# Kernel optimization log

Measured on AMD Instinct MI355X. Metric: run time of the kernel, lower is better.

The kernel has to match this reference:

```python
import jax, jax.numpy as jnp
import numpy as np

NUM_HEAD = 16
D_MODEL = 1024
D_HEAD = D_MODEL // NUM_HEAD
BATCH = 4
SEQ = 2048


def setup_inputs() -> dict:
    key = jax.random.key(0)
    kq, kk, kv, kw, kb = jax.random.split(key, 5)
    Q = jax.random.normal(kq, (BATCH, SEQ, D_MODEL), dtype=jnp.float32)
    K = jax.random.normal(kk, (BATCH, SEQ, D_MODEL), dtype=jnp.float32)
    V = jax.random.normal(kv, (BATCH, SEQ, D_MODEL), dtype=jnp.float32)
    # nn.Linear weight [out, in] and bias [out]; scaled like torch default init
    Wq_w = jax.random.normal(kw, (D_MODEL, D_MODEL), dtype=jnp.float32) * (1.0 / np.sqrt(D_MODEL))
    Wq_b = jax.random.normal(kb, (D_MODEL,), dtype=jnp.float32) * 0.01
    return {"Q": Q, "K": K, "V": V, "Wq_w": Wq_w, "Wq_b": Wq_b}


def _split_head(x):
    # [b, s, d_model] -> [b, h, s, d_head]
    b, s, _ = x.shape
    return x.reshape(b, s, NUM_HEAD, D_HEAD).transpose(0, 2, 1, 3)


def reference(Q, K, V, Wq_w, Wq_b):
    # NOTE: original module (faithfully) uses Wq for all three projections.
    q = Q @ Wq_w.T + Wq_b
    k = K @ Wq_w.T + Wq_b
    v = V @ Wq_w.T + Wq_b
    q = _split_head(q)  # [b, h, s, dh]
    k = _split_head(k)
    v = _split_head(v)
    scale = 1.0 / jnp.sqrt(jnp.float32(D_HEAD))
    scores = jnp.einsum("bhqd,bhkd->bhqk", q, k) * scale  # [b, h, s, s]
    att_w = jax.nn.softmax(scores, axis=-1)
    out = jnp.einsum("bhqk,bhkd->bhqd", att_w, v)
    out = out.transpose(0, 2, 1, 3).reshape(Q.shape[0], -1, D_MODEL)
    return out, att_w
```

## Files before the change

kernel.cpp:

```cpp
#include <hip/hip_runtime.h>

typedef _Float16 f16;
typedef _Float16 f16x8 __attribute__((ext_vector_type(8)));
typedef _Float16 f16x4 __attribute__((ext_vector_type(4)));
typedef float    f32x4 __attribute__((ext_vector_type(4)));

static constexpr int NBATCH = 4;
static constexpr int NH     = 16;
static constexpr int SQ     = 2048;
static constexpr int DM     = 1024;
static constexpr int DHEAD  = 64;
static constexpr size_t TEL = (size_t)NBATCH * SQ * DM;
static constexpr size_t WEL = (size_t)DM * DM;

#define MFMA(a, b, c) __builtin_amdgcn_mfma_f32_16x16x32_f16((a), (b), (c), 0, 0, 0)

#define GLOAD_LDS16(g, l)                                        \
    __builtin_amdgcn_global_load_lds(                            \
        (const __attribute__((address_space(1))) void*)(g),      \
        (__attribute__((address_space(3))) void*)(l), 16, 0, 0)

__global__ __launch_bounds__(256) void cvt_kernel(
    const float* __restrict__ X0, const float* __restrict__ X1,
    const float* __restrict__ X2, const float* __restrict__ W,
    f16* __restrict__ y0, f16* __restrict__ y1,
    f16* __restrict__ y2, f16* __restrict__ yw)
{
    constexpr int CX = (int)(TEL / 8);
    constexpr int CW = (int)(WEL / 8);
    const int total = 3 * CX + CW;
    for (int c = blockIdx.x * blockDim.x + threadIdx.x; c < total;
         c += gridDim.x * blockDim.x) {
        const float* src; f16* dst; int off;
        if (c < CX)            { src = X0; dst = y0; off = c; }
        else if (c < 2 * CX)   { src = X1; dst = y1; off = c - CX; }
        else if (c < 3 * CX)   { src = X2; dst = y2; off = c - 2 * CX; }
        else                   { src = W;  dst = yw; off = c - 3 * CX; }
        const float* p = src + (size_t)off * 8;
        float4 lo = *(const float4*)p;
        float4 hi = *(const float4*)(p + 4);
        f16x8 v;
        v[0] = (f16)lo.x; v[1] = (f16)lo.y; v[2] = (f16)lo.z; v[3] = (f16)lo.w;
        v[4] = (f16)hi.x; v[5] = (f16)hi.y; v[6] = (f16)hi.z; v[7] = (f16)hi.w;
        *(f16x8*)(dst + (size_t)off * 8) = v;
    }
}

__global__ __launch_bounds__(256, 2) void proj_kernel(
    const f16* __restrict__ X0, const f16* __restrict__ X1,
    const f16* __restrict__ X2, const f16* __restrict__ W,
    const float* __restrict__ bias,
    f16* __restrict__ wq, f16* __restrict__ wk, f16* __restrict__ wv)
{
    alignas(16) __shared__ f16 la[2][128 * 32];
    alignas(16) __shared__ f16 lb[2][128 * 32];

    const int bid   = blockIdx.x;
    const int which = bid / 512;
    const int t0    = bid % 512;
    const int nb    = t0 >> 6;
    const int mb    = t0 & 63;
    const f16* __restrict__ X  = (which == 0) ? X0 : (which == 1) ? X1 : X2;
    const f16* __restrict__ A0 = X + (size_t)mb * 128 * DM;
    const f16* __restrict__ B0 = W + (size_t)nb * 128 * DM;

    const int tid  = threadIdx.x;
    const int wave = tid >> 6;
    const int lane = tid & 63;
    const int wr   = wave >> 1, wc = wave & 1;
    const int l16  = lane & 15, g = lane >> 4;
    const int m_base = mb * 128 + wr * 64;
    const int n_base = nb * 128 + wc * 64;

    auto stage = [&](int buf, int k0) {
        #pragma unroll
        for (int half = 0; half < 2; ++half) {
            const int idx = half * 256 + wave * 64 + lane;
            const int row = idx >> 2;
            const int sc  = (idx & 3) ^ ((row >> 1) & 3);
            const int db  = (half * 256 + wave * 64) * 8;
            GLOAD_LDS16(A0 + (size_t)row * DM + k0 + sc * 8, &la[buf][db]);
            GLOAD_LDS16(B0 + (size_t)row * DM + k0 + sc * 8, &lb[buf][db]);
        }
    };

    f32x4 acc[4][4];
    #pragma unroll
    for (int i = 0; i < 4; ++i)
        #pragma unroll
        for (int j = 0; j < 4; ++j)
            acc[i][j] = (f32x4){0.f, 0.f, 0.f, 0.f};

    stage(0, 0);
    __syncthreads();
    for (int t = 0; t < 32; ++t) {
        const int buf = t & 1;
        if (t < 31) stage(buf ^ 1, (t + 1) * 32);
        f16x8 af[4], bf[4];
        #pragma unroll
        for (int qs = 0; qs < 4; ++qs) {
            const int row = wr * 64 + qs * 16 + l16;
            af[qs] = *(const f16x8*)&la[buf][row * 32 +
                                             ((g ^ ((row >> 1) & 3)) << 3)];
        }
        #pragma unroll
        for (int ns = 0; ns < 4; ++ns) {
            const int row = wc * 64 + ns * 16 + l16;
            bf[ns] = *(const f16x8*)&lb[buf][row * 32 +
                                             ((g ^ ((row >> 1) & 3)) << 3)];
        }
        #pragma unroll
        for (int qs = 0; qs < 4; ++qs)
            #pragma unroll
            for (int ns = 0; ns < 4; ++ns)
                acc[qs][ns] = MFMA(af[qs], bf[ns], acc[qs][ns]);
        __syncthreads();
    }

    const int    s_base = m_base & (SQ - 1);
    const int    b      = m_base >> 11;
    const int    h      = nb * 2 + wc;
    const size_t bh     = (size_t)b * NH + h;

    float bv[4];
    #pragma unroll
    for (int ns = 0; ns < 4; ++ns) bv[ns] = bias[n_base + ns * 16 + l16];

    if (which == 2) {
        #pragma unroll
        for (int qs = 0; qs < 4; ++qs)
            #pragma unroll
            for (int ns = 0; ns < 4; ++ns) {
                f16x4 pk;
                #pragma unroll
                for (int r = 0; r < 4; ++r) pk[r] = (f16)(acc[qs][ns][r] + bv[ns]);
                const int dh = ns * 16 + l16;
                const int s0 = s_base + qs * 16 + 4 * g;
                *(f16x4*)(wv + (bh * DHEAD + dh) * SQ + s0) = pk;
            }
    } else {
        f16* __restrict__ dst = (which == 0) ? wq : wk;
        const float sc = (which == 0) ? 0.125f : 1.0f;
        #pragma unroll
        for (int qs = 0; qs < 4; ++qs)
            #pragma unroll
            for (int ns = 0; ns < 4; ++ns)
                #pragma unroll
                for (int r = 0; r < 4; ++r) {
                    const int s  = s_base + qs * 16 + 4 * g + r;
                    const int dh = ns * 16 + l16;
                    dst[(bh * SQ + s) * DHEAD + dh] =
                        (f16)((acc[qs][ns][r] + bv[ns]) * sc);
                }
    }
}

__global__ __launch_bounds__(256, 2) void attn_kernel(
    const f16* __restrict__ wq, const f16* __restrict__ wk,
    const f16* __restrict__ wv,
    float* __restrict__ out, float* __restrict__ att)
{
    alignas(16) __shared__ f16 lk[2][64 * 64];
    alignas(16) __shared__ f16 lv[2][64 * 64];
    alignas(16) __shared__ f16 plds[4][16 * 40];

    const int tid  = threadIdx.x;
    const int wave = tid >> 6;
    const int lane = tid & 63;
    const int l16  = lane & 15, g = lane >> 4;

    const int bid     = blockIdx.x;
    const int logical = (bid & 7) * 128 + (bid >> 3);
    const int bh      = logical >> 4;
    const int q0      = (logical & 15) * 128 + wave * 32;

    const f16* __restrict__ qp = wq + (size_t)bh * SQ * DHEAD;
    const f16* __restrict__ kp = wk + (size_t)bh * SQ * DHEAD;
    const f16* __restrict__ vp = wv + (size_t)bh * DHEAD * SQ;
    float* __restrict__ attp = att + ((size_t)bh * SQ + q0) * SQ;
    const int b = bh >> 4, h = bh & 15;
    float* __restrict__ outp = out + ((size_t)b * SQ + q0) * DM + h * DHEAD;

    auto stage64 = [&](f16* dst0, const f16* gbase, int stride) {
        #pragma unroll
        for (int half = 0; half < 2; ++half) {
            const int idx = half * 256 + wave * 64 + lane;
            const int row = idx >> 3;
            const int sc  = (idx & 7) ^ (row & 7);
            GLOAD_LDS16(gbase + (size_t)row * stride + sc * 8,
                        dst0 + (size_t)(half * 256 + wave * 64) * 8);
        }
    };
    auto ldk8 = [&](int buf, int row, int c) -> f16x8 {
        return *(const f16x8*)&lk[buf][row * 64 + ((c ^ (row & 7)) << 3)];
    };
    auto ldv8 = [&](int buf, int row, int c) -> f16x8 {
        return *(const f16x8*)&lv[buf][row * 64 + ((c ^ (row & 7)) << 3)];
    };

    f16x8 qf[2][2];
    #pragma unroll
    for (int qs = 0; qs < 2; ++qs)
        #pragma unroll
        for (int dhf = 0; dhf < 2; ++dhf)
            qf[qs][dhf] = *(const f16x8*)(qp + (size_t)(q0 + qs * 16 + l16) * DHEAD +
                                          dhf * 32 + g * 8);

    const f32x4 zero = (f32x4){0.f, 0.f, 0.f, 0.f};
    constexpr int NT = SQ / 64;

    float accl[2][4];
    #pragma unroll
    for (int qs = 0; qs < 2; ++qs)
        #pragma unroll
        for (int r = 0; r < 4; ++r) accl[qs][r] = 0.f;

    stage64(&lk[0][0], kp, DHEAD);
    __syncthreads();
    for (int t = 0; t < NT; ++t) {
        const int buf = t & 1;
        if (t + 1 < NT)
            stage64(&lk[buf ^ 1][0], kp + (size_t)(t + 1) * 64 * DHEAD, DHEAD);
        #pragma unroll
        for (int st = 0; st < 4; ++st) {
            const int row = st * 16 + l16;
            f16x8 kf0 = ldk8(buf, row, g);
            f16x8 kf1 = ldk8(buf, row, 4 + g);
            #pragma unroll
            for (int qs = 0; qs < 2; ++qs) {
                f32x4 sc = MFMA(qf[qs][0], kf0, zero);
                sc = MFMA(qf[qs][1], kf1, sc);
                #pragma unroll
                for (int r = 0; r < 4; ++r) accl[qs][r] += __expf(sc[r]);
            }
        }
        __syncthreads();
    }
    #pragma unroll
    for (int qs = 0; qs < 2; ++qs)
        #pragma unroll
        for (int r = 0; r < 4; ++r) {
            float v = accl[qs][r];
            #pragma unroll
            for (int m = 1; m < 16; m <<= 1) v += __shfl_xor(v, m, 64);
            accl[qs][r] = v;
        }
    float linv[2][4];
    #pragma unroll
    for (int qs = 0; qs < 2; ++qs)
        #pragma unroll
        for (int r = 0; r < 4; ++r) linv[qs][r] = 1.f / accl[qs][r];

    f32x4 oacc[2][4];
    #pragma unroll
    for (int qs = 0; qs < 2; ++qs)
        #pragma unroll
        for (int ds = 0; ds < 4; ++ds) oacc[qs][ds] = zero;

    stage64(&lk[0][0], kp, DHEAD);
    stage64(&lv[0][0], vp, SQ);
    __syncthreads();
    for (int t = 0; t < NT; ++t) {
        const int buf = t & 1;
        const int kv0 = t * 64;
        if (t + 1 < NT) {
            stage64(&lk[buf ^ 1][0], kp + (size_t)(t + 1) * 64 * DHEAD, DHEAD);
            stage64(&lv[buf ^ 1][0], vp + (t + 1) * 64, SQ);
        }
        #pragma unroll
        for (int s2 = 0; s2 < 2; ++s2) {
            const int kv = kv0 + s2 * 32;
            f16x8 kf[2][2];
            #pragma unroll
            for (int ks = 0; ks < 2; ++ks) {
                const int row = s2 * 32 + ks * 16 + l16;
                kf[ks][0] = ldk8(buf, row, g);
                kf[ks][1] = ldk8(buf, row, 4 + g);
            }
            float pvv[2][2][4];
            #pragma unroll
            for (int qs = 0; qs < 2; ++qs)
                #pragma unroll
                for (int ks = 0; ks < 2; ++ks) {
                    f32x4 sc = MFMA(qf[qs][0], kf[ks][0], zero);
                    sc = MFMA(qf[qs][1], kf[ks][1], sc);
                    #pragma unroll
                    for (int r = 0; r < 4; ++r)
                        pvv[qs][ks][r] = __expf(sc[r]) * linv[qs][r];
                }
            #pragma unroll
            for (int qs = 0; qs < 2; ++qs)
                #pragma unroll
                for (int ks = 0; ks < 2; ++ks)
                    #pragma unroll
                    for (int r = 0; r < 4; ++r) {
                        const int row = qs * 16 + 4 * g + r;
                        attp[(size_t)row * SQ + kv + ks * 16 + l16] = pvv[qs][ks][r];
                    }
            f16x8 vf[4];
            #pragma unroll
            for (int ds = 0; ds < 4; ++ds)
                vf[ds] = ldv8(buf, ds * 16 + l16, s2 * 4 + g);
            #pragma unroll
            for (int qs = 0; qs < 2; ++qs) {
                #pragma unroll
                for (int ks = 0; ks < 2; ++ks)
                    #pragma unroll
                    for (int r = 0; r < 4; ++r)
                        plds[wave][(4 * g + r) * 40 + ks * 16 + l16] =
                            (f16)pvv[qs][ks][r];
                f16x8 pa = *(const f16x8*)&plds[wave][l16 * 40 + g * 8];
                #pragma unroll
                for (int ds = 0; ds < 4; ++ds)
                    oacc[qs][ds] = MFMA(pa, vf[ds], oacc[qs][ds]);
            }
        }
        __syncthreads();
    }

    #pragma unroll
    for (int qs = 0; qs < 2; ++qs)
        #pragma unroll
        for (int ds = 0; ds < 4; ++ds)
            #pragma unroll
            for (int r = 0; r < 4; ++r)
                outp[(size_t)(qs * 16 + 4 * g + r) * DM + ds * 16 + l16] =
                    oacc[qs][ds][r];
}

extern "C" void kernel_launch(void* const* d_in, const int* in_sizes, int n_in,
                              void* d_out, int out_size, void* d_ws, size_t ws_size,
                              hipStream_t stream) {
    const float* Q    = (const float*)d_in[0];
    const float* K    = (const float*)d_in[1];
    const float* V    = (const float*)d_in[2];
    const float* W    = (const float*)d_in[3];
    const float* bias = (const float*)d_in[4];

    f16* wq = (f16*)d_ws;
    f16* wk = wq + TEL;
    f16* wv = wk + TEL;

    float* out = (float*)d_out;
    float* att = out + TEL;

    f16* x0 = (f16*)att;
    f16* x1 = x0 + TEL;
    f16* x2 = x1 + TEL;
    f16* xw = x2 + TEL;

    cvt_kernel <<<2048, 256, 0, stream>>>(Q, K, V, W, x0, x1, x2, xw);
    proj_kernel<<<1536, 256, 0, stream>>>(x0, x1, x2, xw, bias, wq, wk, wv);
    attn_kernel<<<1024, 256, 0, stream>>>(wq, wk, wv, out, att);
}
```

Before: 487.4 us.

## Defer softmax normalization and transpose score MFMA to drop the LDS round-trip for P

Restructures the attention kernel so the first pass computes unnormalized P@V together with the row sums, then normalizes the output once. A second pass recomputes the scores to write the normalized attention weights as vectorized float4 stores. Computing S transposed (K as the A operand) puts the probabilities directly into the B-operand layout of a 16x16x16 MFMA, which removes the per-wave LDS shuffle buffer. Occupancy hint is raised to 4 blocks per CU; the risks are register pressure and no max subtraction in exp, which the old code also lacked.

```diff
diff --git a/kernel.cpp b/kernel.cpp
--- a/kernel.cpp
+++ b/kernel.cpp
@@ -13,7 +13,8 @@
 static constexpr size_t TEL = (size_t)NBATCH * SQ * DM;
 static constexpr size_t WEL = (size_t)DM * DM;
 
-#define MFMA(a, b, c) __builtin_amdgcn_mfma_f32_16x16x32_f16((a), (b), (c), 0, 0, 0)
+#define MFMA32(a, b, c) __builtin_amdgcn_mfma_f32_16x16x32_f16((a), (b), (c), 0, 0, 0)
+#define MFMA16(a, b, c) __builtin_amdgcn_mfma_f32_16x16x16f16((a), (b), (c), 0, 0, 0)
 
 #define GLOAD_LDS16(g, l)                                        \
     __builtin_amdgcn_global_load_lds(                            \
@@ -113,7 +114,7 @@
         for (int qs = 0; qs < 4; ++qs)
             #pragma unroll
             for (int ns = 0; ns < 4; ++ns)
-                acc[qs][ns] = MFMA(af[qs], bf[ns], acc[qs][ns]);
+                acc[qs][ns] = MFMA32(af[qs], bf[ns], acc[qs][ns]);
         __syncthreads();
     }
 
@@ -155,14 +156,13 @@
     }
 }
 
-__global__ __launch_bounds__(256, 2) void attn_kernel(
+__global__ __launch_bounds__(256, 4) void attn_kernel(
     const f16* __restrict__ wq, const f16* __restrict__ wk,
     const f16* __restrict__ wv,
     float* __restrict__ out, float* __restrict__ att)
 {
     alignas(16) __shared__ f16 lk[2][64 * 64];
     alignas(16) __shared__ f16 lv[2][64 * 64];
-    alignas(16) __shared__ f16 plds[4][16 * 40];
 
     const int tid  = threadIdx.x;
     const int wave = tid >> 6;
@@ -194,8 +194,9 @@
     auto ldk8 = [&](int buf, int row, int c) -> f16x8 {
         return *(const f16x8*)&lk[buf][row * 64 + ((c ^ (row & 7)) << 3)];
     };
-    auto ldv8 = [&](int buf, int row, int c) -> f16x8 {
-        return *(const f16x8*)&lv[buf][row * 64 + ((c ^ (row & 7)) << 3)];
+    auto ldv4 = [&](int buf, int row, int c_lin, int half8) -> f16x4 {
+        return *(const f16x4*)&lv[buf][row * 64 + ((c_lin ^ (row & 7)) << 3) +
+                                       half8 * 4];
     };
 
     f16x8 qf[2][2];
@@ -209,48 +210,7 @@
     const f32x4 zero = (f32x4){0.f, 0.f, 0.f, 0.f};
     constexpr int NT = SQ / 64;
 
-    float accl[2][4];
-    #pragma unroll
-    for (int qs = 0; qs < 2; ++qs)
-        #pragma unroll
-        for (int r = 0; r < 4; ++r) accl[qs][r] = 0.f;
-
-    stage64(&lk[0][0], kp, DHEAD);
-    __syncthreads();
-    for (int t = 0; t < NT; ++t) {
-        const int buf = t & 1;
-        if (t + 1 < NT)
-            stage64(&lk[buf ^ 1][0], kp + (size_t)(t + 1) * 64 * DHEAD, DHEAD);
-        #pragma unroll
-        for (int st = 0; st < 4; ++st) {
-            const int row = st * 16 + l16;
-            f16x8 kf0 = ldk8(buf, row, g);
-            f16x8 kf1 = ldk8(buf, row, 4 + g);
-            #pragma unroll
-            for (int qs = 0; qs < 2; ++qs) {
-                f32x4 sc = MFMA(qf[qs][0], kf0, zero);
-                sc = MFMA(qf[qs][1], kf1, sc);
-                #pragma unroll
-                for (int r = 0; r < 4; ++r) accl[qs][r] += __expf(sc[r]);
-            }
-        }
-        __syncthreads();
-    }
-    #pragma unroll
-    for (int qs = 0; qs < 2; ++qs)
-        #pragma unroll
-        for (int r = 0; r < 4; ++r) {
-            float v = accl[qs][r];
-            #pragma unroll
-            for (int m = 1; m < 16; m <<= 1) v += __shfl_xor(v, m, 64);
-            accl[qs][r] = v;
-        }
-    float linv[2][4];
-    #pragma unroll
-    for (int qs = 0; qs < 2; ++qs)
-        #pragma unroll
-        for (int r = 0; r < 4; ++r) linv[qs][r] = 1.f / accl[qs][r];
-
+    float accl[2] = {0.f, 0.f};
     f32x4 oacc[2][4];
     #pragma unroll
     for (int qs = 0; qs < 2; ++qs)
@@ -262,70 +222,85 @@
     __syncthreads();
     for (int t = 0; t < NT; ++t) {
         const int buf = t & 1;
-        const int kv0 = t * 64;
         if (t + 1 < NT) {
             stage64(&lk[buf ^ 1][0], kp + (size_t)(t + 1) * 64 * DHEAD, DHEAD);
             stage64(&lv[buf ^ 1][0], vp + (t + 1) * 64, SQ);
         }
         #pragma unroll
-        for (int s2 = 0; s2 < 2; ++s2) {
-            const int kv = kv0 + s2 * 32;
-            f16x8 kf[2][2];
-            #pragma unroll
-            for (int ks = 0; ks < 2; ++ks) {
-                const int row = s2 * 32 + ks * 16 + l16;
-                kf[ks][0] = ldk8(buf, row, g);
-                kf[ks][1] = ldk8(buf, row, 4 + g);
+        for (int s16 = 0; s16 < 4; ++s16) {
+            const int row = s16 * 16 + l16;
+            f16x8 kf0 = ldk8(buf, row, g);
+            f16x8 kf1 = ldk8(buf, row, 4 + g);
+            f16x4 pb[2];
+            #pragma unroll
+            for (int qs = 0; qs < 2; ++qs) {
+                f32x4 sc = MFMA32(kf0, qf[qs][0], zero);
+                sc = MFMA32(kf1, qf[qs][1], sc);
+                float e0 = __expf(sc[0]), e1 = __expf(sc[1]);
+                float e2 = __expf(sc[2]), e3 = __expf(sc[3]);
+                accl[qs] += (e0 + e1) + (e2 + e3);
+                f16x4 p; p[0] = (f16)e0; p[1] = (f16)e1;
+                p[2] = (f16)e2; p[3] = (f16)e3;
+                pb[qs] = p;
             }
-            float pvv[2][2][4];
-            #pragma unroll
-            for (int qs = 0; qs < 2; ++qs)
-                #pragma unroll
-                for (int ks = 0; ks < 2; ++ks) {
-                    f32x4 sc = MFMA(qf[qs][0], kf[ks][0], zero);
-                    sc = MFMA(qf[qs][1], kf[ks][1], sc);
-                    #pragma unroll
-                    for (int r = 0; r < 4; ++r)
-                        pvv[qs][ks][r] = __expf(sc[r]) * linv[qs][r];
-                }
-            #pragma unroll
-            for (int qs = 0; qs < 2; ++qs)
-                #pragma unroll
-                for (int ks = 0; ks < 2; ++ks)
-                    #pragma unroll
-                    for (int r = 0; r < 4; ++r) {
-                        const int row = qs * 16 + 4 * g + r;
-                        attp[(size_t)row * SQ + kv + ks * 16 + l16] = pvv[qs][ks][r];
-                    }
-            f16x8 vf[4];
-            #pragma unroll
-            for (int ds = 0; ds < 4; ++ds)
-                vf[ds] = ldv8(buf, ds * 16 + l16, s2 * 4 + g);
+            #pragma unroll
+            for (int ds = 0; ds < 4; ++ds) {
+                f16x4 vf = ldv4(buf, ds * 16 + l16, s16 * 2 + (g >> 1), g & 1);
+                oacc[0][ds] = MFMA16(vf, pb[0], oacc[0][ds]);
+                oacc[1][ds] = MFMA16(vf, pb[1], oacc[1][ds]);
+            }
+        }
+        __syncthreads();
+    }
+
+    float linv[2];
+    #pragma unroll
+    for (int qs = 0; qs < 2; ++qs) {
+        float v = accl[qs];
+        v += __shfl_xor(v, 16, 64);
+        v += __shfl_xor(v, 32, 64);
+        linv[qs] = 1.f / v;
+    }
+
+    #pragma unroll
+    for (int qs = 0; qs < 2; ++qs)
+        #pragma unroll
+        for (int ds = 0; ds < 4; ++ds) {
+            float4 o;
+            o.x = oacc[qs][ds][0] * linv[qs];
+            o.y = oacc[qs][ds][1] * linv[qs];
+            o.z = oacc[qs][ds][2] * linv[qs];
+            o.w = oacc[qs][ds][3] * linv[qs];
+            *(float4*)(outp + (size_t)(qs * 16 + l16) * DM + ds * 16 + 4 * g) = o;
+        }
+
+    stage64(&lk[0][0], kp, DHEAD);
+    __syncthreads();
+    for (int t = 0; t < NT; ++t) {
+        const int buf = t & 1;
+        const int kv0 = t * 64;
+        if (t + 1 < NT)
+            stage64(&lk[buf ^ 1][0], kp + (size_t)(t + 1) * 64 * DHEAD, DHEAD);
+        #pragma unroll
+        for (int s16 = 0; s16 < 4; ++s16) {
+            const int row = s16 * 16 + l16;
+            f16x8 kf0 = ldk8(buf, row, g);
+            f16x8 kf1 = ldk8(buf, row, 4 + g);
             #pragma unroll
             for (int qs = 0; qs < 2; ++qs) {
-                #pragma unroll
-                for (int ks = 0; ks < 2; ++ks)
-                    #pragma unroll
-                    for (int r = 0; r < 4; ++r)
-                        plds[wave][(4 * g + r) * 40 + ks * 16 + l16] =
-                            (f16)pvv[qs][ks][r];
-                f16x8 pa = *(const f16x8*)&plds[wave][l16 * 40 + g * 8];
-                #pragma unroll
-                for (int ds = 0; ds < 4; ++ds)
-                    oacc[qs][ds] = MFMA(pa, vf[ds], oacc[qs][ds]);
+                f32x4 sc = MFMA32(kf0, qf[qs][0], zero);
+                sc = MFMA32(kf1, qf[qs][1], sc);
+                float4 a;
+                a.x = __expf(sc[0]) * linv[qs];
+                a.y = __expf(sc[1]) * linv[qs];
+                a.z = __expf(sc[2]) * linv[qs];
+                a.w = __expf(sc[3]) * linv[qs];
+                *(float4*)(attp + (size_t)(qs * 16 + l16) * SQ + kv0 +
+                           s16 * 16 + 4 * g) = a;
             }
         }
         __syncthreads();
     }
-
-    #pragma unroll
-    for (int qs = 0; qs < 2; ++qs)
-        #pragma unroll
-        for (int ds = 0; ds < 4; ++ds)
-            #pragma unroll
-            for (int r = 0; r < 4; ++r)
-                outp[(size_t)(qs * 16 + 4 * g + r) * DM + ds * 16 + l16] =
-                    oacc[qs][ds][r];
 }
 
 extern "C" void kernel_launch(void* const* d_in, const int* in_sizes, int n_in,
```

After: 442.4 us. -9.2%, faster.
